# Optimization experiments

Hardware: AMD Instinct MI355X
Metric: run time of the kernel (lower is better)

## Reference

```python
import jax, jax.numpy as jnp
import numpy as np

N_ENT = 200_000
N_REL = 500
IN_DIM = 128
OUT_DIM = 128
N_TRIP = 200_000
MARGIN = 6.0
EPSILON = 2.0
REL_RANGE = (MARGIN + EPSILON) / OUT_DIM  # (margin+epsilon)/out_dim
PI = 3.141592653589793
BN_EPS = 1e-5
LRELU_SLOPE = 0.01


def _embed(table, idx, max_norm=1.0):
    # torch nn.Embedding(max_norm=1) renormalizes looked-up rows to norm <= 1
    e = table[idx]
    nrm = jnp.linalg.norm(e, axis=-1, keepdims=True)
    return e * jnp.minimum(1.0, max_norm / jnp.maximum(nrm, 1e-12))


def _bn(x, gamma, beta):
    # BatchNorm1d, training mode (batch stats, biased variance)
    mu = jnp.mean(x, axis=0, keepdims=True)
    var = jnp.var(x, axis=0, keepdims=True)
    return (x - mu) * jax.lax.rsqrt(var + BN_EPS) * gamma + beta


def _rotate(triplets, ent, rel):
    # RotatE distance, mode='head_batch' (raw table indexing as in original)
    h = ent[triplets[:, 0]]
    t = ent[triplets[:, 1]]
    r = rel[triplets[:, 2]]
    re_h, im_h = jnp.split(h, 2, axis=-1)
    re_t, im_t = jnp.split(t, 2, axis=-1)
    # phase dim must match entity half-dim (in_dim//2)
    phase = (r / (REL_RANGE / PI))[:, : IN_DIM // 2]
    re_r, im_r = jnp.cos(phase), jnp.sin(phase)
    re_s = re_r * re_t + im_r * im_t - re_h
    im_s = re_r * im_t - im_r * re_t - im_h
    return jnp.sqrt(re_s * re_s + im_s * im_s).sum(-1)  # [n]


def setup_inputs() -> dict:
    key = jax.random.key(0)
    ks = jax.random.split(key, 8)
    t0 = jax.random.randint(ks[0], (N_TRIP,), 0, N_ENT)
    t1 = jax.random.randint(ks[1], (N_TRIP,), 0, N_ENT)
    t2 = jax.random.randint(ks[2], (N_TRIP,), 0, N_REL)
    triplets = jnp.stack([t0, t1, t2], axis=1)
    ent_embed = jax.random.uniform(ks[3], (N_ENT, IN_DIM), minval=-REL_RANGE, maxval=REL_RANGE, dtype=jnp.float32)
    rel_embed = jax.random.uniform(ks[4], (N_REL, IN_DIM), minval=-REL_RANGE, maxval=REL_RANGE, dtype=jnp.float32)
    # xavier_normal with gain=1.414
    W_a = jax.random.normal(ks[5], (OUT_DIM, 3 * IN_DIM), dtype=jnp.float32) * (1.414 * np.sqrt(2.0 / (3 * IN_DIM + OUT_DIM)))
    b_a = jnp.zeros((OUT_DIM,), jnp.float32)
    W_a2 = jax.random.normal(ks[6], (1, OUT_DIM), dtype=jnp.float32) * (1.414 * np.sqrt(2.0 / (OUT_DIM + 1)))
    b_a2 = jnp.zeros((1,), jnp.float32)
    gamma0 = jnp.ones((3 * IN_DIM,), jnp.float32)
    beta0 = jnp.zeros((3 * IN_DIM,), jnp.float32)
    gamma1 = jnp.ones((OUT_DIM,), jnp.float32)
    beta1 = jnp.zeros((OUT_DIM,), jnp.float32)
    return dict(triplets=triplets, ent_embed=ent_embed, rel_embed=rel_embed,
                W_a=W_a, b_a=b_a, W_a2=W_a2, b_a2=b_a2,
                gamma0=gamma0, beta0=beta0, gamma1=gamma1, beta1=beta1)


def reference(triplets, ent_embed, rel_embed, W_a, b_a, W_a2, b_a2, gamma0, beta0, gamma1, beta1):
    n = triplets.shape[0]
    e0 = _embed(ent_embed, triplets[:, 0])
    e1 = _embed(ent_embed, triplets[:, 1])
    er = _embed(rel_embed, triplets[:, 2])
    h = jnp.concatenate([jnp.concatenate([e0, e1, er], axis=1),
                         jnp.concatenate([e1, e0, -er], axis=1)], axis=0)  # [2n, 3*in_dim]
    h = _bn(h, gamma0, beta0)  # dropout in eval -> identity
    c = _bn(h @ W_a.T + b_a, gamma1, beta1)  # [2n, out_dim]
    s = c @ W_a2.T + b_a2  # [2n, 1]
    b = -jnp.where(s >= 0, s, LRELU_SLOPE * s)
    e_b = jnp.exp(b)  # [2n, 1]
    # edges[0] = cat(t0, t1): scatter-sum over edge targets (KBGAT special spmm)
    tgt = jnp.concatenate([triplets[:, 0], triplets[:, 1]])
    ebs = jax.ops.segment_sum(e_b, tgt, num_segments=N_ENT)  # [N, 1]
    temp1 = e_b * c  # [2n, out_dim]
    hs = jax.ops.segment_sum(temp1, tgt, num_segments=N_ENT)  # [N, out_dim]
    ebs = jnp.where(ebs == 0, 1e-12, ebs)
    h_ent = hs / ebs  # [N, out_dim]
    # per-relation mean of forward-edge messages minus backward-edge messages
    ridx = triplets[:, 2]
    cnt = jnp.maximum(jax.ops.segment_sum(jnp.ones((n,), temp1.dtype), ridx, num_segments=N_REL), 1.0)[:, None]
    h_rel = (jax.ops.segment_sum(temp1[:n], ridx, num_segments=N_REL)
             - jax.ops.segment_sum(temp1[n:], ridx, num_segments=N_REL)) / cnt  # [R, out_dim]
    score = MARGIN - _rotate(triplets, ent_embed, rel_embed)  # [n]
    return h_ent, h_rel, score
```

## Files before the change

### kernel.cpp

```cpp
#include <hip/hip_runtime.h>
#include <stdint.h>

#define N_TRIP 200000
#define N_ENT  200000
#define N_REL  500
#define D      128
#define MARGINF 6.0f
#define BN_EPSF 1e-5f
#define PHASE_C 50.26548245743669f

typedef unsigned short u16;
typedef unsigned int   u32;
typedef unsigned long long u64;
typedef __attribute__((ext_vector_type(8))) short short8;
typedef __attribute__((ext_vector_type(4))) float f32x4;
typedef __attribute__((ext_vector_type(4))) unsigned short u16x4;

__device__ inline float bfl(u32 u){ return __uint_as_float(u<<16); }
__device__ inline float bfh(u32 u){ return __uint_as_float(u&0xffff0000u); }
__device__ inline u16 f2bf(float f){
  u32 u = __float_as_uint(f);
  u32 r = (u + 0x7fffu + ((u>>16)&1u))>>16;
  return (u16)r;
}

__global__ __launch_bounds__(256) void k_hist(const int* __restrict__ trip,
    int* __restrict__ cnt0, int* __restrict__ cnt1, int* __restrict__ cntr){
  __shared__ int rc[N_REL];
  int t = threadIdx.x;
  for(int r=t; r<N_REL; r+=256) rc[r]=0;
  __syncthreads();
  #pragma unroll
  for(int k=0;k<8;k++){
    int i = blockIdx.x*2048 + t + k*256;
    if(i < N_TRIP){
      atomicAdd(&cnt0[trip[3*i]],   1);
      atomicAdd(&cnt1[trip[3*i+1]], 1);
      atomicAdd(&rc[trip[3*i+2]],   1);
    }
  }
  __syncthreads();
  for(int r=t; r<N_REL; r+=256){
    int c = rc[r];
    if(c) atomicAdd(&cntr[r], c);
  }
}

__global__ __launch_bounds__(1024) void k_scan1(const int* __restrict__ cnt0,
    const int* __restrict__ cnt1, int* __restrict__ offs, int* __restrict__ bsum){
  __shared__ int sh[1024];
  int t = threadIdx.x;
  int e = blockIdx.x*1024 + t;
  int d = (e < N_ENT) ? cnt0[e] + cnt1[e] : 0;
  sh[t] = d; __syncthreads();
  for(int st=1; st<1024; st<<=1){
    int x = (t>=st) ? sh[t-st] : 0;
    __syncthreads();
    sh[t] += x;
    __syncthreads();
  }
  if(e < N_ENT) offs[e] = sh[t] - d;
  if(t == 1023) bsum[blockIdx.x] = sh[t];
}

__global__ __launch_bounds__(512) void k_scan2(const int* __restrict__ bsum,
    int* __restrict__ boffs, const int* __restrict__ cntr,
    int* __restrict__ roffs, int* __restrict__ rcur, int nblk){
  __shared__ int sh[512];
  int t = threadIdx.x;
  int v = (t < nblk) ? bsum[t] : 0;
  sh[t] = v; __syncthreads();
  for(int st=1; st<512; st<<=1){
    int x = (t>=st) ? sh[t-st] : 0;
    __syncthreads(); sh[t] += x; __syncthreads();
  }
  if(t < nblk) boffs[t] = sh[t] - v;
  __syncthreads();
  int w = (t < N_REL) ? cntr[t] : 0;
  sh[t] = w; __syncthreads();
  for(int st=1; st<512; st<<=1){
    int x = (t>=st) ? sh[t-st] : 0;
    __syncthreads(); sh[t] += x; __syncthreads();
  }
  if(t < N_REL){ roffs[t] = sh[t]-w; rcur[t] = sh[t]-w; }
}

__global__ __launch_bounds__(1024) void k_scan3(int* __restrict__ offs,
    const int* __restrict__ boffs, int* __restrict__ cur){
  int e = blockIdx.x*1024 + threadIdx.x;
  if(e < N_ENT){
    int o = offs[e] + boffs[blockIdx.x];
    offs[e] = o;
    cur[e] = o;
  }
}

__global__ __launch_bounds__(256) void k_edges(const int* __restrict__ trip,
    int* __restrict__ cur, int* __restrict__ rcur,
    u32* __restrict__ ebuf, u64* __restrict__ pair64, u64* __restrict__ rpair){
  __shared__ int rcnt[N_REL];
  __shared__ int rbase[N_REL];
  int t = threadIdx.x;
  for(int r=t; r<N_REL; r+=256) rcnt[r]=0;
  __syncthreads();
  int i0 = blockIdx.x*2048;
  int lt0[8], lt1[8], lt2[8], lp[8];
  #pragma unroll
  for(int k=0;k<8;k++){
    int i = i0 + t + k*256;
    lt2[k] = -1;
    if(i < N_TRIP){
      int t0 = trip[3*i], t1 = trip[3*i+1], t2 = trip[3*i+2];
      lt0[k]=t0; lt1[k]=t1; lt2[k]=t2;
      lp[k] = atomicAdd(&rcnt[t2], 1);
      pair64[i] = ((u64)t2<<36) | ((u64)t1<<18) | (u64)t0;
      ebuf[atomicAdd(&cur[t0], 1)] = ((u32)t1<<10) | ((u32)t2<<1);
      ebuf[atomicAdd(&cur[t1], 1)] = ((u32)t0<<10) | ((u32)t2<<1) | 1u;
    }
  }
  __syncthreads();
  for(int r=t; r<N_REL; r+=256){
    int c = rcnt[r];
    rbase[r] = c ? atomicAdd(&rcur[r], c) : 0;
  }
  __syncthreads();
  #pragma unroll
  for(int k=0;k<8;k++){
    if(lt2[k] >= 0)
      rpair[rbase[lt2[k]] + lp[k]] =
        ((u64)lt2[k]<<36) | ((u64)lt1[k]<<18) | (u64)lt0[k];
  }
}

__global__ __launch_bounds__(256) void k_prep(const float* __restrict__ ent,
    u32* __restrict__ entnbf, u32* entbf){
  int t = threadIdx.x, lane = t & 63;
  int l16 = lane & 15, g = lane >> 4;
  int wid = blockIdx.x*4 + (t>>6), nw = gridDim.x*4;
  for(int e8 = wid*8; e8 < N_ENT; e8 += nw*8){
    int eA = e8 + g, eB = e8 + 4 + g;
    const float* xpA = ent + (size_t)eA*D + l16*8;
    const float* xpB = ent + (size_t)eB*D + l16*8;
    float4 a0 = *(const float4*)xpA;
    float4 a1 = *(const float4*)(xpA+4);
    float4 b0 = *(const float4*)xpB;
    float4 b1 = *(const float4*)(xpB+4);
    if(entbf){
      uint4 pa, pb;
      pa.x = (u32)f2bf(a0.x) | ((u32)f2bf(a0.y)<<16);
      pa.y = (u32)f2bf(a0.z) | ((u32)f2bf(a0.w)<<16);
      pa.z = (u32)f2bf(a1.x) | ((u32)f2bf(a1.y)<<16);
      pa.w = (u32)f2bf(a1.z) | ((u32)f2bf(a1.w)<<16);
      pb.x = (u32)f2bf(b0.x) | ((u32)f2bf(b0.y)<<16);
      pb.y = (u32)f2bf(b0.z) | ((u32)f2bf(b0.w)<<16);
      pb.z = (u32)f2bf(b1.x) | ((u32)f2bf(b1.y)<<16);
      pb.w = (u32)f2bf(b1.z) | ((u32)f2bf(b1.w)<<16);
      *(uint4*)(entbf + (size_t)eA*64 + l16*4) = pa;
      *(uint4*)(entbf + (size_t)eB*64 + l16*4) = pb;
    }
    float ssA = a0.x*a0.x + a0.y*a0.y + a0.z*a0.z + a0.w*a0.w
              + a1.x*a1.x + a1.y*a1.y + a1.z*a1.z + a1.w*a1.w;
    float ssB = b0.x*b0.x + b0.y*b0.y + b0.z*b0.z + b0.w*b0.w
              + b1.x*b1.x + b1.y*b1.y + b1.z*b1.z + b1.w*b1.w;
    #pragma unroll
    for(int o=8;o>0;o>>=1){
      ssA += __shfl_xor(ssA,o,64);
      ssB += __shfl_xor(ssB,o,64);
    }
    float nA = sqrtf(ssA), nB = sqrtf(ssB);
    float scA = nA > 1.0f ? 1.0f/nA : 1.0f;
    float scB = nB > 1.0f ? 1.0f/nB : 1.0f;
    uint4 na, nb;
    na.x = (u32)f2bf(a0.x*scA) | ((u32)f2bf(a0.y*scA)<<16);
    na.y = (u32)f2bf(a0.z*scA) | ((u32)f2bf(a0.w*scA)<<16);
    na.z = (u32)f2bf(a1.x*scA) | ((u32)f2bf(a1.y*scA)<<16);
    na.w = (u32)f2bf(a1.z*scA) | ((u32)f2bf(a1.w*scA)<<16);
    nb.x = (u32)f2bf(b0.x*scB) | ((u32)f2bf(b0.y*scB)<<16);
    nb.y = (u32)f2bf(b0.z*scB) | ((u32)f2bf(b0.w*scB)<<16);
    nb.z = (u32)f2bf(b1.x*scB) | ((u32)f2bf(b1.y*scB)<<16);
    nb.w = (u32)f2bf(b1.z*scB) | ((u32)f2bf(b1.w*scB)<<16);
    *(uint4*)(entnbf + (size_t)eA*64 + l16*4) = na;
    *(uint4*)(entnbf + (size_t)eB*64 + l16*4) = nb;
  }
}

__global__ __launch_bounds__(256) void k_stats(const u32* __restrict__ entnbf,
    const int* __restrict__ cnt0, const int* __restrict__ cnt1,
    float* __restrict__ stats){
  __shared__ float acc[512];
  int t = threadIdx.x;
  acc[t] = 0.f; acc[t+256] = 0.f;
  __syncthreads();
  int lane = t & 63;
  int l16 = lane & 15, g = lane >> 4;
  int wid = blockIdx.x*4 + (t>>6), nw = gridDim.x*4;
  float s0[8]={0,0,0,0,0,0,0,0}, s1[8]={0,0,0,0,0,0,0,0};
  float q0[8]={0,0,0,0,0,0,0,0}, q1[8]={0,0,0,0,0,0,0,0};
  for(int e4 = wid*4; e4 < N_ENT; e4 += nw*4){
    int e = e4 + g;
    uint4 u = *(const uint4*)(entnbf + (size_t)e*64 + l16*4);
    float w0 = (float)cnt0[e], w1 = (float)cnt1[e];
    float v[8] = {bfl(u.x),bfh(u.x),bfl(u.y),bfh(u.y),
                  bfl(u.z),bfh(u.z),bfl(u.w),bfh(u.w)};
    #pragma unroll
    for(int k=0;k<8;k++){
      s0[k] += w0*v[k]; s1[k] += w1*v[k];
      q0[k] += w0*v[k]*v[k]; q1[k] += w1*v[k]*v[k];
    }
  }
  #pragma unroll
  for(int k=0;k<8;k++){
    int c = l16*8 + k;
    atomicAdd(&acc[c],     s0[k]);
    atomicAdd(&acc[128+c], s1[k]);
    atomicAdd(&acc[256+c], q0[k]);
    atomicAdd(&acc[384+c], q1[k]);
  }
  __syncthreads();
  atomicAdd(&stats[t],     acc[t]);
  atomicAdd(&stats[t+256], acc[t+256]);
}

__global__ __launch_bounds__(256) void k_relstats(const float* __restrict__ rel,
    const int* __restrict__ cntr, float* __restrict__ scale_rel,
    float* __restrict__ stats, float* __restrict__ cosr, float* __restrict__ sinr){
  int t = threadIdx.x, lane = t & 63;
  int r = blockIdx.x*4 + (t>>6);
  if(r >= N_REL) return;
  float2 x = *(const float2*)(rel + (size_t)r*D + 2*lane);
  float ss = x.x*x.x + x.y*x.y;
  #pragma unroll
  for(int o=32;o>0;o>>=1) ss += __shfl_xor(ss,o,64);
  float nrm = sqrtf(ss);
  float sc = nrm > 1.0f ? 1.0f/nrm : 1.0f;
  if(lane==0) scale_rel[r] = sc;
  float w = (float)cntr[r];
  float sx = x.x*sc, sy = x.y*sc;
  atomicAdd(&stats[512 + 2*lane  ], w*sx*sx);
  atomicAdd(&stats[512 + 2*lane+1], w*sy*sy);
  if(lane < 32){
    cosr[r*64 + 2*lane  ] = cosf(x.x*PHASE_C);
    sinr[r*64 + 2*lane  ] = sinf(x.x*PHASE_C);
    cosr[r*64 + 2*lane+1] = cosf(x.y*PHASE_C);
    sinr[r*64 + 2*lane+1] = sinf(x.y*PHASE_C);
  }
}

__global__ __launch_bounds__(384) void k_bn0fin(const float* __restrict__ stats,
    const float* __restrict__ W_a, const float* __restrict__ b_a,
    const float* __restrict__ gamma0, const float* __restrict__ beta0,
    u16* __restrict__ Wbf, float* __restrict__ W2, float* __restrict__ bprime){
  __shared__ float a0[384], c0[384];
  int t = threadIdx.x;
  {
    int j = t & 127;
    float mu, ex2;
    if(t < 256){
      mu  = (stats[j]     + stats[128+j]) * (1.0f/(2.0f*N_TRIP));
      ex2 = (stats[256+j] + stats[384+j]) * (1.0f/(2.0f*N_TRIP));
    } else {
      mu  = 0.0f;
      ex2 = stats[512+j] * (1.0f/N_TRIP);
    }
    float var = ex2 - mu*mu;
    float a = gamma0[t]*rsqrtf(var + BN_EPSF);
    a0[t] = a;
    c0[t] = beta0[t] - mu*a;
  }
  __syncthreads();
  for(int idx=t; idx<256*128; idx+=384){
    int j = idx>>7, k = idx&127;
    int ko = ((j>>7)<<7) + k;
    Wbf[idx] = f2bf(W_a[(j&127)*384 + ko]*a0[ko]);
  }
  for(int idx=t; idx<128*128; idx+=384){
    int k = idx>>7, j = idx&127;
    W2[idx] = W_a[j*384 + 256 + k]*a0[256+k];
  }
  if(t < 128){
    float s = b_a[t];
    for(int k=0;k<384;k++) s += W_a[t*384+k]*c0[k];
    bprime[t] = s;
  }
}

__global__ __launch_bounds__(128) void k_relproj(const float* __restrict__ rel,
    const float* __restrict__ scale_rel, const float* __restrict__ W2,
    float* __restrict__ R){
  int r = blockIdx.x, j = threadIdx.x;
  __shared__ float x[128];
  x[j] = rel[(size_t)r*D + j]*scale_rel[r];
  __syncthreads();
  float s = 0.f;
  for(int k=0;k<128;k++) s += x[k]*W2[k*128+j];
  R[r*128+j] = s;
}

__global__ __launch_bounds__(256) void k_ab(const u32* __restrict__ entnbf,
    const u16* __restrict__ Wbf, u16* __restrict__ Abuf, u16* __restrict__ Bbuf){
  __shared__ u16 xlds[16*128];
  int t = threadIdx.x, lane = t & 63, q = t >> 6;
  int kgrp = (lane>>4)<<3;
  int rgrp = (lane>>4)<<2;
  int frow = lane & 15;
  short8 wf[4][4];
  #pragma unroll
  for(int jt=0;jt<4;jt++){
    #pragma unroll
    for(int kt=0;kt<4;kt++)
      wf[jt][kt] = *(const short8*)(Wbf + (size_t)(q*64 + jt*16 + frow)*D + kgrp + kt*32);
  }
  int srow = t>>4;
  int scol16 = t&15;
  char* swp = (char*)xlds + srow*256 + ((scol16<<4) ^ ((srow&7)<<4));
  const char* rdp = (const char*)xlds + frow*256;
  int rbase0 = (lane>>4)<<4;
  int fsw = (frow&7)<<4;
  for(int chunk = blockIdx.x; chunk < N_ENT/16; chunk += gridDim.x){
    uint4 pk = *(const uint4*)(entnbf + (size_t)(chunk*16 + srow)*64 + scol16*4);
    __syncthreads();
    *(uint4*)swp = pk;
    __syncthreads();
    short8 xf[4];
    #pragma unroll
    for(int kt=0;kt<4;kt++)
      xf[kt] = *(const short8*)(rdp + ((rbase0 + kt*64) ^ fsw));
    int erow = chunk*16 + frow;
    #pragma unroll
    for(int jt=0;jt<4;jt++){
      f32x4 acc = {0.f,0.f,0.f,0.f};
      #pragma unroll
      for(int kt=0;kt<4;kt++)
        acc = __builtin_amdgcn_mfma_f32_16x16x32_bf16(wf[jt][kt], xf[kt], acc, 0,0,0);
      int jbase = q*64 + jt*16 + rgrp;
      u16x4 opk;
      opk.x=f2bf(acc[0]); opk.y=f2bf(acc[1]); opk.z=f2bf(acc[2]); opk.w=f2bf(acc[3]);
      u16* dst = (jbase < 128) ? (Abuf + (size_t)erow*D + jbase)
                               : (Bbuf + (size_t)erow*D + (jbase-128));
      *(u16x4*)dst = opk;
    }
  }
}

__global__ __launch_bounds__(256) void k_bn1stats(const u64* __restrict__ pair64,
    const u16* __restrict__ A, const u16* __restrict__ B,
    const float* __restrict__ R, const float* __restrict__ bprime,
    float* __restrict__ sums){
  __shared__ float acc[256];
  int t = threadIdx.x;
  acc[t] = 0.f;
  __syncthreads();
  int lane = t & 63;
  int gw = blockIdx.x*4 + (t>>6), nw = gridDim.x*4;
  float bp0 = bprime[2*lane], bp1 = bprime[2*lane+1];
  float s0=0,s1=0,q0=0,q1=0;
  for(int i=4*gw; i<N_TRIP; i+=8*nw){
    {
      u64 pr = pair64[i];
      int t0 = (int)(pr & 0x3FFFF);
      int t1 = (int)((pr>>18) & 0x3FFFF);
      int t2 = (int)(pr>>36);
      u32 ua0 = *(const u32*)(A + (size_t)t0*D + 2*lane);
      u32 ua1 = *(const u32*)(A + (size_t)t1*D + 2*lane);
      u32 ub0 = *(const u32*)(B + (size_t)t0*D + 2*lane);
      u32 ub1 = *(const u32*)(B + (size_t)t1*D + 2*lane);
      float2 r = *(const float2*)(R + (size_t)t2*D + 2*lane);
      float y1x = bfl(ua0)+bfl(ub1)+r.x+bp0;
      float y1y = bfh(ua0)+bfh(ub1)+r.y+bp1;
      float y2x = bfl(ua1)+bfl(ub0)-r.x+bp0;
      float y2y = bfh(ua1)+bfh(ub0)-r.y+bp1;
      s0 += y1x+y2x; s1 += y1y+y2y;
      q0 += y1x*y1x + y2x*y2x; q1 += y1y*y1y + y2y*y2y;
    }
    int i2 = i + 4*nw;
    if(i2 < N_TRIP){
      u64 pr = pair64[i2];
      int t0 = (int)(pr & 0x3FFFF);
      int t1 = (int)((pr>>18) & 0x3FFFF);
      int t2 = (int)(pr>>36);
      u32 ua0 = *(const u32*)(A + (size_t)t0*D + 2*lane);
      u32 ua1 = *(const u32*)(A + (size_t)t1*D + 2*lane);
      u32 ub0 = *(const u32*)(B + (size_t)t0*D + 2*lane);
      u32 ub1 = *(const u32*)(B + (size_t)t1*D + 2*lane);
      float2 r = *(const float2*)(R + (size_t)t2*D + 2*lane);
      float y1x = bfl(ua0)+bfl(ub1)+r.x+bp0;
      float y1y = bfh(ua0)+bfh(ub1)+r.y+bp1;
      float y2x = bfl(ua1)+bfl(ub0)-r.x+bp0;
      float y2y = bfh(ua1)+bfh(ub0)-r.y+bp1;
      s0 += y1x+y2x; s1 += y1y+y2y;
      q0 += y1x*y1x + y2x*y2x; q1 += y1y*y1y + y2y*y2y;
    }
  }
  atomicAdd(&acc[      2*lane  ], s0);
  atomicAdd(&acc[      2*lane+1], s1);
  atomicAdd(&acc[128 + 2*lane  ], q0);
  atomicAdd(&acc[128 + 2*lane+1], q1);
  __syncthreads();
  atomicAdd(&sums[t], acc[t]);
}

__global__ __launch_bounds__(128) void k_bn1fin(const float* __restrict__ sums,
    const float* __restrict__ gamma1, const float* __restrict__ beta1,
    const float* __restrict__ W_a2, const float* __restrict__ b_a2,
    const float* __restrict__ bprime, float* __restrict__ a1c){
  __shared__ float red[128];
  int j = threadIdx.x;
  float mu  = sums[j]    *(2.0f/(float)N_TRIP);
  float var = sums[128+j]*(2.0f/(float)N_TRIP) - mu*mu;
  float a = gamma1[j]*rsqrtf(var + BN_EPSF);
  float cc = beta1[j] - mu*a;
  float wa1 = W_a2[j]*a;
  a1c[j]     = a;
  a1c[128+j] = cc;
  a1c[256+j] = wa1;
  red[j] = W_a2[j]*cc + wa1*bprime[j];
  __syncthreads();
  #pragma unroll
  for(int s=64; s>0; s>>=1){
    if(j < s) red[j] += red[j+s];
    __syncthreads();
  }
  if(j==0) a1c[384] = red[0] + b_a2[0];
}

__global__ __launch_bounds__(256) void k_alphabeta(const u16* __restrict__ A,
    const u16* __restrict__ B, const float* __restrict__ R,
    const float* __restrict__ a1c, float* __restrict__ alpha,
    float* __restrict__ beta, float* __restrict__ rho){
  int t = threadIdx.x, lane = t & 63;
  int l32 = lane & 31, grp = lane >> 5;
  int wid = blockIdx.x*4 + (t>>6), nw = gridDim.x*4;
  float4 wa = *(const float4*)(a1c + 256 + l32*4);
  for(int e4 = wid*4; e4 < N_ENT; e4 += nw*4){
    int eA = e4 + grp, eB = e4 + 2 + grp;
    uint2 uaA = *(const uint2*)(A + (size_t)eA*D + l32*4);
    uint2 ubA = *(const uint2*)(B + (size_t)eA*D + l32*4);
    uint2 uaB = *(const uint2*)(A + (size_t)eB*D + l32*4);
    uint2 ubB = *(const uint2*)(B + (size_t)eB*D + l32*4);
    float daA = wa.x*bfl(uaA.x) + wa.y*bfh(uaA.x) + wa.z*bfl(uaA.y) + wa.w*bfh(uaA.y);
    float dbA = wa.x*bfl(ubA.x) + wa.y*bfh(ubA.x) + wa.z*bfl(ubA.y) + wa.w*bfh(ubA.y);
    float daB = wa.x*bfl(uaB.x) + wa.y*bfh(uaB.x) + wa.z*bfl(uaB.y) + wa.w*bfh(uaB.y);
    float dbB = wa.x*bfl(ubB.x) + wa.y*bfh(ubB.x) + wa.z*bfl(ubB.y) + wa.w*bfh(ubB.y);
    #pragma unroll
    for(int o=16;o>0;o>>=1){
      daA += __shfl_xor(daA,o,64); dbA += __shfl_xor(dbA,o,64);
      daB += __shfl_xor(daB,o,64); dbB += __shfl_xor(dbB,o,64);
    }
    if(l32==0){ alpha[eA]=daA; beta[eA]=dbA; alpha[eB]=daB; beta[eB]=dbB; }
  }
  for(int r2 = wid*2 + grp; r2 < N_REL; r2 += nw*2){
    float4 rr = *(const float4*)(R + (size_t)r2*D + l32*4);
    float dr = wa.x*rr.x + wa.y*rr.y + wa.z*rr.z + wa.w*rr.w;
    #pragma unroll
    for(int o=16;o>0;o>>=1) dr += __shfl_xor(dr,o,64);
    if(l32==0) rho[r2]=dr;
  }
}

__global__ __launch_bounds__(256) void k_ent(
    const int* __restrict__ offs, const int* __restrict__ endp,
    const u32* __restrict__ ebuf,
    const u16* __restrict__ A, const u16* __restrict__ B,
    const float* __restrict__ R, const float* __restrict__ bprime,
    const float* __restrict__ a1c, const float* __restrict__ alpha,
    const float* __restrict__ beta, const float* __restrict__ rho,
    float* __restrict__ out_hent){
  int t = threadIdx.x, lane = t & 63;
  int l16 = lane & 15, g = lane >> 4;
  int wid = blockIdx.x*4 + (t>>6), nw = gridDim.x*4;
  int cb = l16*8;
  float4 bpA = *(const float4*)(bprime + cb);
  float4 bpB = *(const float4*)(bprime + cb + 4);
  float4 a1A = *(const float4*)(a1c + cb);
  float4 a1B = *(const float4*)(a1c + cb + 4);
  float4 ccA = *(const float4*)(a1c + 128 + cb);
  float4 ccB = *(const float4*)(a1c + 128 + cb + 4);
  float kap = a1c[384];
  for(int e4 = wid*4; e4 < N_ENT; e4 += nw*4){
    int e = e4 + g;
    int s = offs[e], en = endp[e];
    uint4 ua = *(const uint4*)(A + (size_t)e*D + cb);
    float ax0 = bfl(ua.x), ax1 = bfh(ua.x), ax2 = bfl(ua.y), ax3 = bfh(ua.y);
    float ax4 = bfl(ua.z), ax5 = bfh(ua.z), ax6 = bfl(ua.w), ax7 = bfh(ua.w);
    float al = alpha[e];
    float h0=0,h1=0,h2=0,h3=0,h4=0,h5=0,h6=0,h7=0, eb=0;
    int o = s;
    for(; o+1<en; o+=2){
      u32 idX = ebuf[o], idY = ebuf[o+1];
      int otX = idX>>10, r2X = (idX>>1)&511;
      int otY = idY>>10, r2Y = (idY>>1)&511;
      float sgX = (idX&1) ? -1.f : 1.f;
      float sgY = (idY&1) ? -1.f : 1.f;
      uint4 ubX = *(const uint4*)(B + (size_t)otX*D + cb);
      uint4 ubY = *(const uint4*)(B + (size_t)otY*D + cb);
      float4 rAX = *(const float4*)(R + (size_t)r2X*D + cb);
      float4 rBX = *(const float4*)(R + (size_t)r2X*D + cb + 4);
      float4 rAY = *(const float4*)(R + (size_t)r2Y*D + cb);
      float4 rBY = *(const float4*)(R + (size_t)r2Y*D + cb + 4);
      float beX = beta[otX], beY = beta[otY];
      float roX = rho[r2X],  roY = rho[r2Y];
      float svX = al + beX + sgX*roX + kap;
      float svY = al + beY + sgY*roY + kap;
      float ebX = expf(svX >= 0.f ? -svX : -0.01f*svX);
      float ebY = expf(svY >= 0.f ? -svY : -0.01f*svY);
      float y, c;
      y = ax0 + bfl(ubX.x) + sgX*rAX.x + bpA.x; c = y*a1A.x + ccA.x; h0 += ebX*c;
      y = ax1 + bfh(ubX.x) + sgX*rAX.y + bpA.y; c = y*a1A.y + ccA.y; h1 += ebX*c;
      y = ax2 + bfl(ubX.y) + sgX*rAX.z + bpA.z; c = y*a1A.z + ccA.z; h2 += ebX*c;
      y = ax3 + bfh(ubX.y) + sgX*rAX.w + bpA.w; c = y*a1A.w + ccA.w; h3 += ebX*c;
      y = ax4 + bfl(ubX.z) + sgX*rBX.x + bpB.x; c = y*a1B.x + ccB.x; h4 += ebX*c;
      y = ax5 + bfh(ubX.z) + sgX*rBX.y + bpB.y; c = y*a1B.y + ccB.y; h5 += ebX*c;
      y = ax6 + bfl(ubX.w) + sgX*rBX.z + bpB.z; c = y*a1B.z + ccB.z; h6 += ebX*c;
      y = ax7 + bfh(ubX.w) + sgX*rBX.w + bpB.w; c = y*a1B.w + ccB.w; h7 += ebX*c;
      y = ax0 + bfl(ubY.x) + sgY*rAY.x + bpA.x; c = y*a1A.x + ccA.x; h0 += ebY*c;
      y = ax1 + bfh(ubY.x) + sgY*rAY.y + bpA.y; c = y*a1A.y + ccA.y; h1 += ebY*c;
      y = ax2 + bfl(ubY.y) + sgY*rAY.z + bpA.z; c = y*a1A.z + ccA.z; h2 += ebY*c;
      y = ax3 + bfh(ubY.y) + sgY*rAY.w + bpA.w; c = y*a1A.w + ccA.w; h3 += ebY*c;
      y = ax4 + bfl(ubY.z) + sgY*rBY.x + bpB.x; c = y*a1B.x + ccB.x; h4 += ebY*c;
      y = ax5 + bfh(ubY.z) + sgY*rBY.y + bpB.y; c = y*a1B.y + ccB.y; h5 += ebY*c;
      y = ax6 + bfl(ubY.w) + sgY*rBY.z + bpB.z; c = y*a1B.z + ccB.z; h6 += ebY*c;
      y = ax7 + bfh(ubY.w) + sgY*rBY.w + bpB.w; c = y*a1B.w + ccB.w; h7 += ebY*c;
      eb += ebX + ebY;
    }
    if(o < en){
      u32 id = ebuf[o];
      int ot = id>>10, r2 = (id>>1)&511;
      float sg = (id&1) ? -1.f : 1.f;
      uint4 ub = *(const uint4*)(B + (size_t)ot*D + cb);
      float4 rA = *(const float4*)(R + (size_t)r2*D + cb);
      float4 rB = *(const float4*)(R + (size_t)r2*D + cb + 4);
      float sv = al + beta[ot] + sg*rho[r2] + kap;
      float e_b = expf(sv >= 0.f ? -sv : -0.01f*sv);
      float y, c;
      y = ax0 + bfl(ub.x) + sg*rA.x + bpA.x; c = y*a1A.x + ccA.x; h0 += e_b*c;
      y = ax1 + bfh(ub.x) + sg*rA.y + bpA.y; c = y*a1A.y + ccA.y; h1 += e_b*c;
      y = ax2 + bfl(ub.y) + sg*rA.z + bpA.z; c = y*a1A.z + ccA.z; h2 += e_b*c;
      y = ax3 + bfh(ub.y) + sg*rA.w + bpA.w; c = y*a1A.w + ccA.w; h3 += e_b*c;
      y = ax4 + bfl(ub.z) + sg*rB.x + bpB.x; c = y*a1B.x + ccB.x; h4 += e_b*c;
      y = ax5 + bfh(ub.z) + sg*rB.y + bpB.y; c = y*a1B.y + ccB.y; h5 += e_b*c;
      y = ax6 + bfl(ub.w) + sg*rB.z + bpB.z; c = y*a1B.z + ccB.z; h6 += e_b*c;
      y = ax7 + bfh(ub.w) + sg*rB.w + bpB.w; c = y*a1B.w + ccB.w; h7 += e_b*c;
      eb += e_b;
    }
    float inv = (en > s) ? 1.0f/eb : 0.0f;
    float4 o0; o0.x=h0*inv; o0.y=h1*inv; o0.z=h2*inv; o0.w=h3*inv;
    float4 o1; o1.x=h4*inv; o1.y=h5*inv; o1.z=h6*inv; o1.w=h7*inv;
    *(float4*)(out_hent + (size_t)e*D + cb)     = o0;
    *(float4*)(out_hent + (size_t)e*D + cb + 4) = o1;
  }
}

__global__ __launch_bounds__(512) void k_rel(
    const int* __restrict__ roffs, const int* __restrict__ cntr,
    const u64* __restrict__ rpair,
    const u16* __restrict__ A, const u16* __restrict__ B,
    const float* __restrict__ R, const float* __restrict__ bprime,
    const float* __restrict__ a1c, const float* __restrict__ alpha,
    const float* __restrict__ beta, const float* __restrict__ rho,
    float* __restrict__ out_hrel){
  __shared__ float red[8][128];
  int t = threadIdx.x, lane = t & 63, w = t >> 6;
  int r = blockIdx.x;
  int cnt = cntr[r], base = roffs[r];
  float2 rr = *(const float2*)(R + (size_t)r*D + 2*lane);
  float bp0 = bprime[2*lane], bp1 = bprime[2*lane+1];
  float a1x = a1c[2*lane],     a1y = a1c[2*lane+1];
  float ccx = a1c[128+2*lane], ccy = a1c[128+2*lane+1];
  float kap = a1c[384];
  float rhor = rho[r];
  float sx = 0.f, sy = 0.f;
  for(int j=w; j<cnt; j+=16){
    {
      u64 pr = rpair[base+j];
      int t0 = (int)(pr & 0x3FFFF);
      int t1 = (int)((pr>>18) & 0x3FFFF);
      float s1 = alpha[t0] + beta[t1] + rhor + kap;
      float s2 = alpha[t1] + beta[t0] - rhor + kap;
      float e1 = expf(s1 >= 0.f ? -s1 : -0.01f*s1);
      float e2 = expf(s2 >= 0.f ? -s2 : -0.01f*s2);
      u32 ua0 = *(const u32*)(A + (size_t)t0*D + 2*lane);
      u32 ua1 = *(const u32*)(A + (size_t)t1*D + 2*lane);
      u32 ub0 = *(const u32*)(B + (size_t)t0*D + 2*lane);
      u32 ub1 = *(const u32*)(B + (size_t)t1*D + 2*lane);
      float y1x = bfl(ua0)+bfl(ub1)+rr.x+bp0;
      float y1y = bfh(ua0)+bfh(ub1)+rr.y+bp1;
      float y2x = bfl(ua1)+bfl(ub0)-rr.x+bp0;
      float y2y = bfh(ua1)+bfh(ub0)-rr.y+bp1;
      float c1x = y1x*a1x+ccx, c1y = y1y*a1y+ccy;
      float c2x = y2x*a1x+ccx, c2y = y2y*a1y+ccy;
      sx += e1*c1x - e2*c2x;
      sy += e1*c1y - e2*c2y;
    }
    int j2 = j + 8;
    if(j2 < cnt){
      u64 pr = rpair[base+j2];
      int t0 = (int)(pr & 0x3FFFF);
      int t1 = (int)((pr>>18) & 0x3FFFF);
      float s1 = alpha[t0] + beta[t1] + rhor + kap;
      float s2 = alpha[t1] + beta[t0] - rhor + kap;
      float e1 = expf(s1 >= 0.f ? -s1 : -0.01f*s1);
      float e2 = expf(s2 >= 0.f ? -s2 : -0.01f*s2);
      u32 ua0 = *(const u32*)(A + (size_t)t0*D + 2*lane);
      u32 ua1 = *(const u32*)(A + (size_t)t1*D + 2*lane);
      u32 ub0 = *(const u32*)(B + (size_t)t0*D + 2*lane);
      u32 ub1 = *(const u32*)(B + (size_t)t1*D + 2*lane);
      float y1x = bfl(ua0)+bfl(ub1)+rr.x+bp0;
      float y1y = bfh(ua0)+bfh(ub1)+rr.y+bp1;
      float y2x = bfl(ua1)+bfl(ub0)-rr.x+bp0;
      float y2y = bfh(ua1)+bfh(ub0)-rr.y+bp1;
      float c1x = y1x*a1x+ccx, c1y = y1y*a1y+ccy;
      float c2x = y2x*a1x+ccx, c2y = y2y*a1y+ccy;
      sx += e1*c1x - e2*c2x;
      sy += e1*c1y - e2*c2y;
    }
  }
  float2 p; p.x = sx; p.y = sy;
  *(float2*)&red[w][2*lane] = p;
  __syncthreads();
  if(t < 128){
    float s = 0.f;
    #pragma unroll
    for(int k=0;k<8;k++) s += red[k][t];
    float cf = cnt > 0 ? (float)cnt : 1.0f;
    out_hrel[(size_t)r*D + t] = s/cf;
  }
}

__global__ __launch_bounds__(256) void k_score_bf(const u64* __restrict__ pair64,
    const u32* __restrict__ entbf, const float* __restrict__ cosr,
    const float* __restrict__ sinr, float* __restrict__ score){
  int t = threadIdx.x, lane = t & 63;
  int l16 = lane & 15, g = lane >> 4;
  int wid = blockIdx.x*4 + (t>>6), nw = gridDim.x*4;
  for(int i4 = wid*4; i4 < N_TRIP; i4 += nw*4){
    int i = i4 + g;
    u64 pr = pair64[i];
    int t0 = (int)(pr & 0x3FFFF);
    int t1 = (int)((pr>>18) & 0x3FFFF);
    int t2 = (int)(pr>>36);
    uint2 reh = *(const uint2*)(entbf + (size_t)t0*64 + l16*2);
    uint2 imh = *(const uint2*)(entbf + (size_t)t0*64 + 32 + l16*2);
    uint2 ret = *(const uint2*)(entbf + (size_t)t1*64 + l16*2);
    uint2 imt = *(const uint2*)(entbf + (size_t)t1*64 + 32 + l16*2);
    float4 cr = *(const float4*)(cosr + (size_t)t2*64 + l16*4);
    float4 sr = *(const float4*)(sinr + (size_t)t2*64 + l16*4);
    float rh[4] = {bfl(reh.x),bfh(reh.x),bfl(reh.y),bfh(reh.y)};
    float ih[4] = {bfl(imh.x),bfh(imh.x),bfl(imh.y),bfh(imh.y)};
    float rt[4] = {bfl(ret.x),bfh(ret.x),bfl(ret.y),bfh(ret.y)};
    float it[4] = {bfl(imt.x),bfh(imt.x),bfl(imt.y),bfh(imt.y)};
    float cc[4] = {cr.x,cr.y,cr.z,cr.w};
    float ss[4] = {sr.x,sr.y,sr.z,sr.w};
    float d = 0.f;
    #pragma unroll
    for(int k=0;k<4;k++){
      float res = cc[k]*rt[k] + ss[k]*it[k] - rh[k];
      float ims = cc[k]*it[k] - ss[k]*rt[k] - ih[k];
      d += sqrtf(res*res + ims*ims);
    }
    #pragma unroll
    for(int o=8;o>0;o>>=1) d += __shfl_xor(d,o,64);
    if(l16==0) score[i] = MARGINF - d;
  }
}

__global__ __launch_bounds__(256) void k_score_fp(const u64* __restrict__ pair64,
    const float* __restrict__ ent, const float* __restrict__ cosr,
    const float* __restrict__ sinr, float* __restrict__ score){
  int t = threadIdx.x, lane = t & 63;
  int gw = blockIdx.x*4 + (t>>6), nw = gridDim.x*4;
  for(int i=gw; i<N_TRIP; i+=nw){
    u64 pr = pair64[i];
    int t0 = (int)(pr & 0x3FFFF);
    int t1 = (int)((pr>>18) & 0x3FFFF);
    int t2 = (int)(pr>>36);
    float re_h = ent[(size_t)t0*D + lane];
    float im_h = ent[(size_t)t0*D + 64 + lane];
    float re_t = ent[(size_t)t1*D + lane];
    float im_t = ent[(size_t)t1*D + 64 + lane];
    float cr = cosr[t2*64 + lane], sr = sinr[t2*64 + lane];
    float re_s = cr*re_t + sr*im_t - re_h;
    float im_s = cr*im_t - sr*re_t - im_h;
    float d = sqrtf(re_s*re_s + im_s*im_s);
    #pragma unroll
    for(int o=32;o>0;o>>=1) d += __shfl_xor(d,o,64);
    if(lane==0) score[i] = MARGINF - d;
  }
}

extern "C" void kernel_launch(void* const* d_in, const int* in_sizes, int n_in,
                              void* d_out, int out_size, void* d_ws, size_t ws_size,
                              hipStream_t stream){
  const int*   trip   = (const int*)  d_in[0];
  const float* ent    = (const float*)d_in[1];
  const float* rel    = (const float*)d_in[2];
  const float* W_a    = (const float*)d_in[3];
  const float* b_a    = (const float*)d_in[4];
  const float* W_a2   = (const float*)d_in[5];
  const float* b_a2   = (const float*)d_in[6];
  const float* gamma0 = (const float*)d_in[7];
  const float* beta0  = (const float*)d_in[8];
  const float* gamma1 = (const float*)d_in[9];
  const float* beta1  = (const float*)d_in[10];

  char* ws = (char*)d_ws;
  size_t off = 0;
  auto take = [&](size_t bytes)->void*{
    void* p = ws + off;
    off += (bytes + 255) & ~(size_t)255;
    return p;
  };
  int*   cnt0    = (int*)  take((size_t)N_ENT*4);
  int*   cnt1    = (int*)  take((size_t)N_ENT*4);
  int*   cntr    = (int*)  take((size_t)N_REL*4);
  float* stats   = (float*)take(640*4);
  float* sums    = (float*)take(256*4);
  size_t zero_bytes = off;
  int*   offs      = (int*)  take((size_t)N_ENT*4);
  int*   cur       = (int*)  take((size_t)N_ENT*4);
  int*   bsum      = (int*)  take(512*4);
  int*   boffs     = (int*)  take(512*4);
  int*   roffs     = (int*)  take(512*4);
  int*   rcur      = (int*)  take(512*4);
  u32*   ebuf      = (u32*)  take((size_t)2*N_TRIP*4);
  u64*   pair64    = (u64*)  take((size_t)N_TRIP*8);
  u64*   rpair     = (u64*)  take((size_t)N_TRIP*8);
  float* scale_rel = (float*)take((size_t)N_REL*4);
  u16*   Wbf       = (u16*)  take(256*128*2);
  float* W2        = (float*)take(128*128*4);
  float* bprime    = (float*)take(128*4);
  float* a1c       = (float*)take(512*4);
  float* R         = (float*)take((size_t)N_REL*D*4);
  float* cosr      = (float*)take((size_t)N_REL*64*4);
  float* sinr      = (float*)take((size_t)N_REL*64*4);
  float* alpha     = (float*)take((size_t)N_ENT*4);
  float* betab     = (float*)take((size_t)N_ENT*4);
  float* rho       = (float*)take(512*4);
  u16*   Abuf      = (u16*)  take((size_t)N_ENT*D*2);
  u16*   Bbuf      = (u16*)  take((size_t)N_ENT*D*2);
  u32*   entnbf    = (u32*)  take((size_t)N_ENT*64*4);
  u32*   entbf     = (u32*)  take((size_t)N_ENT*64*4);
  bool use_bf = (off <= ws_size);
  (void)n_in; (void)in_sizes; (void)out_size;

  float* out_hent  = (float*)d_out;
  float* out_hrel  = out_hent + (size_t)N_ENT*D;
  float* out_score = out_hrel + (size_t)N_REL*D;

  hipMemsetAsync(d_ws, 0, zero_bytes, stream);

  const int SCAN_BLKS = (N_ENT + 1023)/1024;
  const int EDG_BLKS  = (N_TRIP + 2047)/2048;
  k_prep     <<<2048, 256, 0, stream>>>(ent, entnbf, use_bf ? entbf : (u32*)nullptr);
  k_hist     <<<EDG_BLKS, 256, 0, stream>>>(trip, cnt0, cnt1, cntr);
  k_scan1    <<<SCAN_BLKS, 1024, 0, stream>>>(cnt0, cnt1, offs, bsum);
  k_scan2    <<<1, 512, 0, stream>>>(bsum, boffs, cntr, roffs, rcur, SCAN_BLKS);
  k_scan3    <<<SCAN_BLKS, 1024, 0, stream>>>(offs, boffs, cur);
  k_edges    <<<EDG_BLKS, 256, 0, stream>>>(trip, cur, rcur, ebuf, pair64, rpair);
  k_stats    <<<640, 256, 0, stream>>>(entnbf, cnt0, cnt1, stats);
  k_relstats <<<(N_REL+3)/4, 256, 0, stream>>>(rel, cntr, scale_rel, stats, cosr, sinr);
  k_bn0fin   <<<1, 384, 0, stream>>>(stats, W_a, b_a, gamma0, beta0, Wbf, W2, bprime);
  k_relproj  <<<N_REL, 128, 0, stream>>>(rel, scale_rel, W2, R);
  k_ab       <<<2048, 256, 0, stream>>>(entnbf, Wbf, Abuf, Bbuf);
  k_bn1stats <<<2048, 256, 0, stream>>>(pair64, Abuf, Bbuf, R, bprime, sums);
  k_bn1fin   <<<1, 128, 0, stream>>>(sums, gamma1, beta1, W_a2, b_a2, bprime, a1c);
  k_alphabeta<<<2048, 256, 0, stream>>>(Abuf, Bbuf, R, a1c, alpha, betab, rho);
  k_ent      <<<2048, 256, 0, stream>>>(offs, cur, ebuf, Abuf, Bbuf, R,
                                        bprime, a1c, alpha, betab, rho, out_hent);
  k_rel      <<<N_REL, 512, 0, stream>>>(roffs, cntr, rpair, Abuf, Bbuf, R,
                                         bprime, a1c, alpha, betab, rho, out_hrel);
  if(use_bf)
    k_score_bf<<<2048, 256, 0, stream>>>(pair64, entbf, cosr, sinr, out_score);
  else
    k_score_fp<<<2048, 256, 0, stream>>>(pair64, ent, cosr, sinr, out_score);
}
```

Before: 454.1 us.

## Fuse BN0 stats into prep kernel and use deterministic per-block partial reductions

The entity batch-norm statistics pass is folded into the prep kernel, which now runs after the histogram so it can weight rows by edge counts. This removes a second full read of the normalized entity table. Global float atomics for the BN0 and BN1 statistics are replaced by per-block partial buffers, reduced by a single-block kernel or inside the BN1 finalize. Grid sizes shrink to 384 and 240 blocks, and relstats accumulates in shared memory before issuing global atomics. The cost is an extra small launch, a serial reduction loop in one block, and possibly less parallelism in prep.

```diff
diff --git a/kernel.cpp b/kernel.cpp
--- a/kernel.cpp
+++ b/kernel.cpp
@@ -8,6 +8,8 @@
 #define MARGINF 6.0f
 #define BN_EPSF 1e-5f
 #define PHASE_C 50.26548245743669f
+#define PREP_BLKS 384
+#define BN1_BLKS  240
 
 typedef unsigned short u16;
 typedef unsigned int   u32;
@@ -133,10 +135,17 @@
 }
 
 __global__ __launch_bounds__(256) void k_prep(const float* __restrict__ ent,
-    u32* __restrict__ entnbf, u32* entbf){
-  int t = threadIdx.x, lane = t & 63;
+    const int* __restrict__ cnt0, const int* __restrict__ cnt1,
+    u32* __restrict__ entnbf, u32* entbf, float* __restrict__ pstat){
+  __shared__ float acc[512];
+  int t = threadIdx.x;
+  acc[t] = 0.f; acc[t+256] = 0.f;
+  __syncthreads();
+  int lane = t & 63;
   int l16 = lane & 15, g = lane >> 4;
   int wid = blockIdx.x*4 + (t>>6), nw = gridDim.x*4;
+  float s0[8]={0,0,0,0,0,0,0,0}, s1[8]={0,0,0,0,0,0,0,0};
+  float q0[8]={0,0,0,0,0,0,0,0}, q1[8]={0,0,0,0,0,0,0,0};
   for(int e8 = wid*8; e8 < N_ENT; e8 += nw*8){
     int eA = e8 + g, eB = e8 + 4 + g;
     const float* xpA = ent + (size_t)eA*D + l16*8;
@@ -170,42 +179,29 @@
     float nA = sqrtf(ssA), nB = sqrtf(ssB);
     float scA = nA > 1.0f ? 1.0f/nA : 1.0f;
     float scB = nB > 1.0f ? 1.0f/nB : 1.0f;
+    float vA[8] = {a0.x*scA,a0.y*scA,a0.z*scA,a0.w*scA,
+                   a1.x*scA,a1.y*scA,a1.z*scA,a1.w*scA};
+    float vB[8] = {b0.x*scB,b0.y*scB,b0.z*scB,b0.w*scB,
+                   b1.x*scB,b1.y*scB,b1.z*scB,b1.w*scB};
     uint4 na, nb;
-    na.x = (u32)f2bf(a0.x*scA) | ((u32)f2bf(a0.y*scA)<<16);
-    na.y = (u32)f2bf(a0.z*scA) | ((u32)f2bf(a0.w*scA)<<16);
-    na.z = (u32)f2bf(a1.x*scA) | ((u32)f2bf(a1.y*scA)<<16);
-    na.w = (u32)f2bf(a1.z*scA) | ((u32)f2bf(a1.w*scA)<<16);
-    nb.x = (u32)f2bf(b0.x*scB) | ((u32)f2bf(b0.y*scB)<<16);
-    nb.y = (u32)f2bf(b0.z*scB) | ((u32)f2bf(b0.w*scB)<<16);
-    nb.z = (u32)f2bf(b1.x*scB) | ((u32)f2bf(b1.y*scB)<<16);
-    nb.w = (u32)f2bf(b1.z*scB) | ((u32)f2bf(b1.w*scB)<<16);
+    na.x = (u32)f2bf(vA[0]) | ((u32)f2bf(vA[1])<<16);
+    na.y = (u32)f2bf(vA[2]) | ((u32)f2bf(vA[3])<<16);
+    na.z = (u32)f2bf(vA[4]) | ((u32)f2bf(vA[5])<<16);
+    na.w = (u32)f2bf(vA[6]) | ((u32)f2bf(vA[7])<<16);
+    nb.x = (u32)f2bf(vB[0]) | ((u32)f2bf(vB[1])<<16);
+    nb.y = (u32)f2bf(vB[2]) | ((u32)f2bf(vB[3])<<16);
+    nb.z = (u32)f2bf(vB[4]) | ((u32)f2bf(vB[5])<<16);
+    nb.w = (u32)f2bf(vB[6]) | ((u32)f2bf(vB[7])<<16);
     *(uint4*)(entnbf + (size_t)eA*64 + l16*4) = na;
     *(uint4*)(entnbf + (size_t)eB*64 + l16*4) = nb;
-  }
-}
-
-__global__ __launch_bounds__(256) void k_stats(const u32* __restrict__ entnbf,
-    const int* __restrict__ cnt0, const int* __restrict__ cnt1,
-    float* __restrict__ stats){
-  __shared__ float acc[512];
-  int t = threadIdx.x;
-  acc[t] = 0.f; acc[t+256] = 0.f;
-  __syncthreads();
-  int lane = t & 63;
-  int l16 = lane & 15, g = lane >> 4;
-  int wid = blockIdx.x*4 + (t>>6), nw = gridDim.x*4;
-  float s0[8]={0,0,0,0,0,0,0,0}, s1[8]={0,0,0,0,0,0,0,0};
-  float q0[8]={0,0,0,0,0,0,0,0}, q1[8]={0,0,0,0,0,0,0,0};
-  for(int e4 = wid*4; e4 < N_ENT; e4 += nw*4){
-    int e = e4 + g;
-    uint4 u = *(const uint4*)(entnbf + (size_t)e*64 + l16*4);
-    float w0 = (float)cnt0[e], w1 = (float)cnt1[e];
-    float v[8] = {bfl(u.x),bfh(u.x),bfl(u.y),bfh(u.y),
-                  bfl(u.z),bfh(u.z),bfl(u.w),bfh(u.w)};
+    float wA0 = (float)cnt0[eA], wA1 = (float)cnt1[eA];
+    float wB0 = (float)cnt0[eB], wB1 = (float)cnt1[eB];
     #pragma unroll
     for(int k=0;k<8;k++){
-      s0[k] += w0*v[k]; s1[k] += w1*v[k];
-      q0[k] += w0*v[k]*v[k]; q1[k] += w1*v[k]*v[k];
+      s0[k] += wA0*vA[k] + wB0*vB[k];
+      s1[k] += wA1*vA[k] + wB1*vB[k];
+      q0[k] += wA0*vA[k]*vA[k] + wB0*vB[k]*vB[k];
+      q1[k] += wA1*vA[k]*vA[k] + wB1*vB[k]*vB[k];
     }
   }
   #pragma unroll
@@ -217,33 +213,47 @@
     atomicAdd(&acc[384+c], q1[k]);
   }
   __syncthreads();
-  atomicAdd(&stats[t],     acc[t]);
-  atomicAdd(&stats[t+256], acc[t+256]);
+  pstat[(size_t)blockIdx.x*512 + t]       = acc[t];
+  pstat[(size_t)blockIdx.x*512 + 256 + t] = acc[t+256];
+}
+
+__global__ __launch_bounds__(512) void k_redstats(const float* __restrict__ pstat,
+    float* __restrict__ stats){
+  int j = threadIdx.x;
+  float s = 0.f;
+  for(int b=0;b<PREP_BLKS;b++) s += pstat[(size_t)b*512 + j];
+  stats[j] = s;
 }
 
 __global__ __launch_bounds__(256) void k_relstats(const float* __restrict__ rel,
     const int* __restrict__ cntr, float* __restrict__ scale_rel,
     float* __restrict__ stats, float* __restrict__ cosr, float* __restrict__ sinr){
+  __shared__ float qacc[128];
   int t = threadIdx.x, lane = t & 63;
+  if(t < 128) qacc[t] = 0.f;
+  __syncthreads();
   int r = blockIdx.x*4 + (t>>6);
-  if(r >= N_REL) return;
-  float2 x = *(const float2*)(rel + (size_t)r*D + 2*lane);
-  float ss = x.x*x.x + x.y*x.y;
-  #pragma unroll
-  for(int o=32;o>0;o>>=1) ss += __shfl_xor(ss,o,64);
-  float nrm = sqrtf(ss);
-  float sc = nrm > 1.0f ? 1.0f/nrm : 1.0f;
-  if(lane==0) scale_rel[r] = sc;
-  float w = (float)cntr[r];
-  float sx = x.x*sc, sy = x.y*sc;
-  atomicAdd(&stats[512 + 2*lane  ], w*sx*sx);
-  atomicAdd(&stats[512 + 2*lane+1], w*sy*sy);
-  if(lane < 32){
-    cosr[r*64 + 2*lane  ] = cosf(x.x*PHASE_C);
-    sinr[r*64 + 2*lane  ] = sinf(x.x*PHASE_C);
-    cosr[r*64 + 2*lane+1] = cosf(x.y*PHASE_C);
-    sinr[r*64 + 2*lane+1] = sinf(x.y*PHASE_C);
-  }
+  if(r < N_REL){
+    float2 x = *(const float2*)(rel + (size_t)r*D + 2*lane);
+    float ss = x.x*x.x + x.y*x.y;
+    #pragma unroll
+    for(int o=32;o>0;o>>=1) ss += __shfl_xor(ss,o,64);
+    float nrm = sqrtf(ss);
+    float sc = nrm > 1.0f ? 1.0f/nrm : 1.0f;
+    if(lane==0) scale_rel[r] = sc;
+    float w = (float)cntr[r];
+    float sx = x.x*sc, sy = x.y*sc;
+    atomicAdd(&qacc[2*lane  ], w*sx*sx);
+    atomicAdd(&qacc[2*lane+1], w*sy*sy);
+    if(lane < 32){
+      cosr[r*64 + 2*lane  ] = cosf(x.x*PHASE_C);
+      sinr[r*64 + 2*lane  ] = sinf(x.x*PHASE_C);
+      cosr[r*64 + 2*lane+1] = cosf(x.y*PHASE_C);
+      sinr[r*64 + 2*lane+1] = sinf(x.y*PHASE_C);
+    }
+  }
+  __syncthreads();
+  if(t < 128) atomicAdd(&stats[512+t], qacc[t]);
 }
 
 __global__ __launch_bounds__(384) void k_bn0fin(const float* __restrict__ stats,
@@ -345,7 +355,7 @@
 __global__ __launch_bounds__(256) void k_bn1stats(const u64* __restrict__ pair64,
     const u16* __restrict__ A, const u16* __restrict__ B,
     const float* __restrict__ R, const float* __restrict__ bprime,
-    float* __restrict__ sums){
+    float* __restrict__ pstat1){
   __shared__ float acc[256];
   int t = threadIdx.x;
   acc[t] = 0.f;
@@ -396,17 +406,22 @@
   atomicAdd(&acc[128 + 2*lane  ], q0);
   atomicAdd(&acc[128 + 2*lane+1], q1);
   __syncthreads();
-  atomicAdd(&sums[t], acc[t]);
-}
-
-__global__ __launch_bounds__(128) void k_bn1fin(const float* __restrict__ sums,
+  pstat1[(size_t)blockIdx.x*256 + t] = acc[t];
+}
+
+__global__ __launch_bounds__(128) void k_bn1fin(const float* __restrict__ pstat1,
     const float* __restrict__ gamma1, const float* __restrict__ beta1,
     const float* __restrict__ W_a2, const float* __restrict__ b_a2,
     const float* __restrict__ bprime, float* __restrict__ a1c){
   __shared__ float red[128];
   int j = threadIdx.x;
-  float mu  = sums[j]    *(2.0f/(float)N_TRIP);
-  float var = sums[128+j]*(2.0f/(float)N_TRIP) - mu*mu;
+  float s = 0.f, q = 0.f;
+  for(int b=0;b<BN1_BLKS;b++){
+    s += pstat1[(size_t)b*256 + j];
+    q += pstat1[(size_t)b*256 + 128 + j];
+  }
+  float mu  = s*(2.0f/(float)N_TRIP);
+  float var = q*(2.0f/(float)N_TRIP) - mu*mu;
   float a = gamma1[j]*rsqrtf(var + BN_EPSF);
   float cc = beta1[j] - mu*a;
   float wa1 = W_a2[j]*a;
@@ -416,8 +431,8 @@
   red[j] = W_a2[j]*cc + wa1*bprime[j];
   __syncthreads();
   #pragma unroll
-  for(int s=64; s>0; s>>=1){
-    if(j < s) red[j] += red[j+s];
+  for(int st=64; st>0; st>>=1){
+    if(j < st) red[j] += red[j+st];
     __syncthreads();
   }
   if(j==0) a1c[384] = red[0] + b_a2[0];
@@ -713,7 +728,6 @@
   int*   cnt1    = (int*)  take((size_t)N_ENT*4);
   int*   cntr    = (int*)  take((size_t)N_REL*4);
   float* stats   = (float*)take(640*4);
-  float* sums    = (float*)take(256*4);
   size_t zero_bytes = off;
   int*   offs      = (int*)  take((size_t)N_ENT*4);
   int*   cur       = (int*)  take((size_t)N_ENT*4);
@@ -735,6 +749,8 @@
   float* alpha     = (float*)take((size_t)N_ENT*4);
   float* betab     = (float*)take((size_t)N_ENT*4);
   float* rho       = (float*)take(512*4);
+  float* pstat     = (float*)take((size_t)PREP_BLKS*512*4);
+  float* pstat1    = (float*)take((size_t)BN1_BLKS*256*4);
   u16*   Abuf      = (u16*)  take((size_t)N_ENT*D*2);
   u16*   Bbuf      = (u16*)  take((size_t)N_ENT*D*2);
   u32*   entnbf    = (u32*)  take((size_t)N_ENT*64*4);
@@ -750,19 +766,20 @@
 
   const int SCAN_BLKS = (N_ENT + 1023)/1024;
   const int EDG_BLKS  = (N_TRIP + 2047)/2048;
-  k_prep     <<<2048, 256, 0, stream>>>(ent, entnbf, use_bf ? entbf : (u32*)nullptr);
   k_hist     <<<EDG_BLKS, 256, 0, stream>>>(trip, cnt0, cnt1, cntr);
+  k_prep     <<<PREP_BLKS, 256, 0, stream>>>(ent, cnt0, cnt1, entnbf,
+                                             use_bf ? entbf : (u32*)nullptr, pstat);
+  k_redstats <<<1, 512, 0, stream>>>(pstat, stats);
   k_scan1    <<<SCAN_BLKS, 1024, 0, stream>>>(cnt0, cnt1, offs, bsum);
   k_scan2    <<<1, 512, 0, stream>>>(bsum, boffs, cntr, roffs, rcur, SCAN_BLKS);
   k_scan3    <<<SCAN_BLKS, 1024, 0, stream>>>(offs, boffs, cur);
   k_edges    <<<EDG_BLKS, 256, 0, stream>>>(trip, cur, rcur, ebuf, pair64, rpair);
-  k_stats    <<<640, 256, 0, stream>>>(entnbf, cnt0, cnt1, stats);
   k_relstats <<<(N_REL+3)/4, 256, 0, stream>>>(rel, cntr, scale_rel, stats, cosr, sinr);
   k_bn0fin   <<<1, 384, 0, stream>>>(stats, W_a, b_a, gamma0, beta0, Wbf, W2, bprime);
   k_relproj  <<<N_REL, 128, 0, stream>>>(rel, scale_rel, W2, R);
   k_ab       <<<2048, 256, 0, stream>>>(entnbf, Wbf, Abuf, Bbuf);
-  k_bn1stats <<<2048, 256, 0, stream>>>(pair64, Abuf, Bbuf, R, bprime, sums);
-  k_bn1fin   <<<1, 128, 0, stream>>>(sums, gamma1, beta1, W_a2, b_a2, bprime, a1c);
+  k_bn1stats <<<BN1_BLKS, 256, 0, stream>>>(pair64, Abuf, Bbuf, R, bprime, pstat1);
+  k_bn1fin   <<<1, 128, 0, stream>>>(pstat1, gamma1, beta1, W_a2, b_a2, bprime, a1c);
   k_alphabeta<<<2048, 256, 0, stream>>>(Abuf, Bbuf, R, a1c, alpha, betab, rho);
   k_ent      <<<2048, 256, 0, stream>>>(offs, cur, ebuf, Abuf, Bbuf, R,
                                         bprime, a1c, alpha, betab, rho, out_hent);
```

New measurement: 426.7 us. -6.0%, faster.
